# Kernel tuning notes

Measured on AMD Instinct MI355X. Metric: run time of the kernel, lower is better.

Reference implementation:

```python
import jax, jax.numpy as jnp
import numpy as np

EMB_DIM = 512
N_HEAD = 8
HEAD_DIM = EMB_DIM // N_HEAD
SEQ_LEN = 2048
BATCH = 4


def setup_inputs() -> dict:
    key = jax.random.key(0)
    k1, k2, k3 = jax.random.split(key, 3)
    emb = jax.random.normal(k1, (SEQ_LEN, BATCH, EMB_DIM), dtype=jnp.float32)
    # torch Linear weight layout: (out_features, in_features)
    W = jax.random.normal(k2, (3 * EMB_DIM, EMB_DIM), dtype=jnp.float32) * 0.02
    b = jax.random.normal(k3, (3 * EMB_DIM,), dtype=jnp.float32) * 0.02
    return {"emb": emb, "W": W, "b": b}


def reference(emb, W, b):
    L, B, E = emb.shape
    scaling = (E / N_HEAD) ** -0.5
    # qkv projection: (L, B, 3E)
    ft = jnp.einsum('lbe,oe->lbo', emb, W) + b
    # interleaved per-head qkv split, matching reshape(L, B*nh, -1).chunk(3, -1)
    ft = ft.reshape(L, B * N_HEAD, 3 * HEAD_DIM).transpose(1, 0, 2)  # (B*nh, L, 3*hd)
    q, k, v = jnp.split(ft, 3, axis=-1)  # each (B*nh, L, hd)
    # attention scores with value-based zero mask
    scores = jnp.einsum('bld,bmd->blm', q, k) * scaling  # (B*nh, L, L)
    mask = scores == 0
    scores = jnp.where(mask, -jnp.inf, scores)
    attn = jax.nn.softmax(scores, axis=-1)
    attn = jnp.where(mask, jnp.zeros((), attn.dtype), attn)
    out = jnp.einsum('blm,bmd->bld', attn, v)  # (B*nh, L, hd)
    out = out.transpose(1, 0, 2).reshape(L, B, E)
    return out
```

## Files before the change

kernel.cpp:

```cpp
#include <hip/hip_runtime.h>
#include <hip/hip_bf16.h>
#include <cstdint>
#include <math.h>


typedef __bf16 bf16x8 __attribute__((ext_vector_type(8)));
typedef float  f32x4  __attribute__((ext_vector_type(4)));
typedef float  f32x16 __attribute__((ext_vector_type(16)));
typedef unsigned int uint32x4 __attribute__((ext_vector_type(4)));

#define MFMA16(a, b, c) __builtin_amdgcn_mfma_f32_16x16x32_bf16(a, b, c, 0, 0, 0)
#define MFMA32(a, b, c) __builtin_amdgcn_mfma_f32_32x32x16_bf16(a, b, c, 0, 0, 0)

#define EXP2F(x) __builtin_amdgcn_exp2f(x)

#define QSCALE 0.18033688011112042f

enum {
  LSEQ = 2048,
  NBATCH = 4,
  EMB = 512,
  NHEAD = 8,
  HDIM = 64,
  NBH = NBATCH * NHEAD,
  MROWS = LSEQ * NBATCH,
  KDIM = EMB,
  NOUT = 3 * EMB
};

__device__ inline void gload_lds16(const void* g, void* l) {
  __builtin_amdgcn_global_load_lds(
      (__attribute__((address_space(1))) void*)(uintptr_t)g,
      (__attribute__((address_space(3))) void*)(uint32_t)(uintptr_t)l,
      16, 0, 0);
}

__device__ inline unsigned packbf(float a, float b) {
  unsigned short ua = __builtin_bit_cast(unsigned short, (__bf16)a);
  unsigned short ub = __builtin_bit_cast(unsigned short, (__bf16)b);
  return (unsigned)ua | ((unsigned)ub << 16);
}

__device__ inline bf16x8 frag_from(unsigned w0, unsigned w1, unsigned w2, unsigned w3) {
  uint32x4 v = {w0, w1, w2, w3};
  return __builtin_bit_cast(bf16x8, v);
}

__global__ __launch_bounds__(256) void cvt_bf16_kernel(const float* __restrict__ in,
                                                       __bf16* __restrict__ out,
                                                       int n8) {
  int i = blockIdx.x * 256 + threadIdx.x;
  if (i >= n8) return;
  const float4* p = (const float4*)in + (size_t)i * 2;
  float4 a = p[0], b = p[1];
  bf16x8 o;
  o[0] = (__bf16)a.x; o[1] = (__bf16)a.y; o[2] = (__bf16)a.z; o[3] = (__bf16)a.w;
  o[4] = (__bf16)b.x; o[5] = (__bf16)b.y; o[6] = (__bf16)b.z; o[7] = (__bf16)b.w;
  *(bf16x8*)(out + (size_t)i * 8) = o;
}

__global__ __launch_bounds__(256) void qkv_gemm_kernel(
    const __bf16* __restrict__ A, const __bf16* __restrict__ Bt,
    const float* __restrict__ bias,
    __bf16* __restrict__ Qh, __bf16* __restrict__ Kh, __bf16* __restrict__ Vth) {
  __shared__ __align__(16) __bf16 As[128 * 64];
  __shared__ __align__(16) __bf16 Bs[128 * 64];

  const int tid = threadIdx.x;
  const int wid = tid >> 6, lane = tid & 63;
  const int g = lane >> 4, lx = lane & 15;
  const int mtile = blockIdx.y, ntile = blockIdx.x;
  const int wm = (wid >> 1) * 64, wn = (wid & 1) * 64;

  const int lr = lane >> 3;
  const int lc = (lane & 7) * 8;

  f32x4 acc[4][4] = {};

  const int rowA0 = mtile * 128;
  const int rowB0 = ntile * 128;

  for (int k0 = 0; k0 < KDIM; k0 += 64) {
#pragma unroll
    for (int i = 0; i < 4; ++i) {
      int chunk = wid * 4 + i;
      gload_lds16(A + (size_t)(rowA0 + chunk * 8 + lr) * KDIM + k0 + lc,
                  As + chunk * 512);
      gload_lds16(Bt + (size_t)(rowB0 + chunk * 8 + lr) * KDIM + k0 + lc,
                  Bs + chunk * 512);
    }
    __syncthreads();
#pragma unroll
    for (int kk = 0; kk < 2; ++kk) {
      bf16x8 af[4], bfr[4];
#pragma unroll
      for (int t = 0; t < 4; ++t)
        af[t] = *(const bf16x8*)&As[(wm + t * 16 + lx) * 64 + kk * 32 + g * 8];
#pragma unroll
      for (int t = 0; t < 4; ++t)
        bfr[t] = *(const bf16x8*)&Bs[(wn + t * 16 + lx) * 64 + kk * 32 + g * 8];
#pragma unroll
      for (int mi = 0; mi < 4; ++mi)
#pragma unroll
        for (int ni = 0; ni < 4; ++ni)
          acc[mi][ni] = MFMA16(af[mi], bfr[ni], acc[mi][ni]);
    }
    __syncthreads();
  }

#pragma unroll
  for (int ni = 0; ni < 4; ++ni) {
    int o = ntile * 128 + wn + ni * 16 + lx;
    float bv = bias[o];
    unsigned h = (unsigned)o / 192u;
    unsigned w = (unsigned)o - h * 192u;
#pragma unroll
    for (int mi = 0; mi < 4; ++mi) {
#pragma unroll
      for (int r = 0; r < 4; ++r) {
        int m = mtile * 128 + wm + mi * 16 + g * 4 + r;
        int l = m >> 2, b = m & 3;
        float v = acc[mi][ni][r] + bv;
        int bh = b * NHEAD + (int)h;
        if (w < 64u) {
          Qh[((size_t)bh * LSEQ + l) * HDIM + w] = (__bf16)(v * QSCALE);
        } else if (w < 128u) {
          Kh[((size_t)bh * LSEQ + l) * HDIM + (w - 64u)] = (__bf16)v;
        } else {
          Vth[((size_t)bh * HDIM + (w - 128u)) * LSEQ + l] = (__bf16)v;
        }
      }
    }
  }
}

__global__ __launch_bounds__(512, 4) void attn_kernel(const __bf16* __restrict__ Qh,
                                                      const __bf16* __restrict__ Kh,
                                                      const __bf16* __restrict__ Vth,
                                                      float* __restrict__ out) {
  __shared__ __align__(16) __bf16 Ks[4][64 * 64];
  __shared__ __align__(16) __bf16 Vs[4][64 * 64];

  const int flat = blockIdx.x;
  const int sw = (flat & 7) * 64 + (flat >> 3);
  const int bh = sw >> 4, qt = sw & 15;
  const int tid = threadIdx.x, wid = tid >> 6, lane = tid & 63;
  const int pair = wid >> 1, role = wid & 1;
  const int ql = lane & 31, hi = lane >> 5;
  const int rb = ql & 7;

  const __bf16* Kb = Kh + (size_t)bh * (LSEQ * HDIM);
  const __bf16* Vb = Vth + (size_t)bh * (HDIM * LSEQ);

  const __bf16* Qp =
      Qh + ((size_t)bh * LSEQ + qt * 128 + pair * 32 + ql) * HDIM + hi * 8;
  bf16x8 qf[4];
#pragma unroll
  for (int s = 0; s < 4; ++s) qf[s] = *(const bf16x8*)(Qp + s * 16);

  const int w4 = wid & 3;
  const int tsel = wid >> 2;
  const int r8 = lane >> 3;
  const int colS = ((lane & 7) ^ r8) * 8;
  const __bf16* pK = Kb + (size_t)(w4 * 16 + r8) * HDIM + colS;
  const __bf16* pV = Vb + (size_t)(w4 * 16 + r8) * LSEQ + colS;

#define STAGE_SS(ss)                                                  \
  do {                                                                \
    int t_ = (2 * (ss) + tsel) & 31;                                  \
    int b_ = t_ & 3;                                                  \
    gload_lds16(pK + (size_t)t_ * (64 * HDIM), &Ks[b_][(w4 * 16) * 64]);      \
    gload_lds16(pK + (size_t)t_ * (64 * HDIM) + 512, &Ks[b_][(w4 * 16 + 8) * 64]); \
    gload_lds16(pV + t_ * 64, &Vs[b_][(w4 * 16) * 64]);               \
    gload_lds16(pV + t_ * 64 + 8 * LSEQ, &Vs[b_][(w4 * 16 + 8) * 64]); \
  } while (0)

  f32x16 ot[2] = {};
  f32x16 lacc = {};

  STAGE_SS(0);
  STAGE_SS(1);
  asm volatile("s_waitcnt vmcnt(4)" ::: "memory");
  __builtin_amdgcn_s_barrier();
  asm volatile("" ::: "memory");

  for (int s = 0; s < 16; ++s) {
    const int cur = (2 * s + role) & 3;

    f32x16 st[2] = {};
    __builtin_amdgcn_s_setprio(1);
#pragma unroll
    for (int kt = 0; kt < 2; ++kt) {
      const __bf16* kr = &Ks[cur][(kt * 32 + ql) * 64];
#pragma unroll
      for (int fs = 0; fs < 4; ++fs) {
        bf16x8 kf = *(const bf16x8*)(kr + (((2 * fs + hi) ^ rb) << 3));
        st[kt] = MFMA32(kf, qf[fs], st[kt]);
      }
    }
    __builtin_amdgcn_s_setprio(0);

#pragma unroll
    for (int r = 0; r < 16; ++r) {
      float e0 = EXP2F(st[0][r]);
      float e1 = EXP2F(st[1][r]);
      st[0][r] = e0;
      st[1][r] = e1;
      lacc[r] += e0 + e1;
    }

    bf16x8 pf[4];
#pragma unroll
    for (int kt = 0; kt < 2; ++kt)
#pragma unroll
      for (int h2 = 0; h2 < 2; ++h2) {
        unsigned a0 = packbf(st[kt][8 * h2 + 0], st[kt][8 * h2 + 1]);
        unsigned a1 = packbf(st[kt][8 * h2 + 2], st[kt][8 * h2 + 3]);
        unsigned a2 = packbf(st[kt][8 * h2 + 4], st[kt][8 * h2 + 5]);
        unsigned a3 = packbf(st[kt][8 * h2 + 6], st[kt][8 * h2 + 7]);
        asm("v_permlane32_swap_b32 %0, %1" : "+v"(a0), "+v"(a2));
        asm("v_permlane32_swap_b32 %0, %1" : "+v"(a1), "+v"(a3));
        pf[kt * 2 + h2] = frag_from(a0, a1, a2, a3);
      }

    __builtin_amdgcn_s_setprio(1);
#pragma unroll
    for (int dt = 0; dt < 2; ++dt) {
      const __bf16* vr = &Vs[cur][(dt * 32 + ql) * 64];
#pragma unroll
      for (int fs = 0; fs < 4; ++fs) {
        bf16x8 vf = *(const bf16x8*)(vr + (((2 * fs + hi) ^ rb) << 3));
        ot[dt] = MFMA32(vf, pf[fs], ot[dt]);
      }
    }
    __builtin_amdgcn_s_setprio(0);

    asm volatile("" ::: "memory");
    __builtin_amdgcn_s_barrier();
    asm volatile("" ::: "memory");
    STAGE_SS(s + 2);
    asm volatile("s_waitcnt vmcnt(4)" ::: "memory");
    __builtin_amdgcn_s_barrier();
    asm volatile("" ::: "memory");
  }
#undef STAGE_SS

  float ls = 0.f;
#pragma unroll
  for (int r = 0; r < 16; ++r) ls += lacc[r];
  ls += __shfl_xor(ls, 32);

  __syncthreads();
  float* stash_ot = (float*)&Ks[0][0];
  float* stash_ls = (float*)&Vs[0][0];
  float* myo = stash_ot + (wid * 64 + lane) * 16;
  f32x16 give = role ? ot[0] : ot[1];
#pragma unroll
  for (int g4 = 0; g4 < 4; ++g4) {
    float4 v4 = make_float4(give[4 * g4 + 0], give[4 * g4 + 1],
                            give[4 * g4 + 2], give[4 * g4 + 3]);
    *(float4*)(myo + 4 * g4) = v4;
  }
  stash_ls[wid * 64 + lane] = ls;
  __syncthreads();

  const float* po = stash_ot + ((wid ^ 1) * 64 + lane) * 16;
  f32x16 mine = role ? ot[1] : ot[0];
#pragma unroll
  for (int r = 0; r < 16; ++r) mine[r] += po[r];
  const float lst = ls + stash_ls[(wid ^ 1) * 64 + lane];
  const float inv = 1.f / lst;

  const int lq = qt * 128 + pair * 32 + ql;
  float* ob = out + (size_t)lq * (NBATCH * EMB) + (bh >> 3) * EMB + (bh & 7) * HDIM;
#pragma unroll
  for (int g4 = 0; g4 < 4; ++g4) {
    float4 v4 = make_float4(mine[4 * g4 + 0] * inv, mine[4 * g4 + 1] * inv,
                            mine[4 * g4 + 2] * inv, mine[4 * g4 + 3] * inv);
    *(float4*)(ob + role * 32 + g4 * 8 + hi * 4) = v4;
  }
}

extern "C" void kernel_launch(void* const* d_in, const int* in_sizes, int n_in,
                              void* d_out, int out_size, void* d_ws, size_t ws_size,
                              hipStream_t stream) {
  const float* emb = (const float*)d_in[0];
  const float* W = (const float*)d_in[1];
  const float* bias = (const float*)d_in[2];
  float* out = (float*)d_out;

  char* ws = (char*)d_ws;
  __bf16* embh = (__bf16*)(ws);
  __bf16* Wh   = (__bf16*)(ws + 8388608);
  __bf16* Qh   = (__bf16*)(ws + 9961472);
  __bf16* Kh   = (__bf16*)(ws + 18350080);
  __bf16* Vth  = (__bf16*)(ws + 26738688);

  cvt_bf16_kernel<<<dim3(MROWS * KDIM / 8 / 256), dim3(256), 0, stream>>>(emb, embh,
                                                                          MROWS * KDIM / 8);
  cvt_bf16_kernel<<<dim3(NOUT * KDIM / 8 / 256), dim3(256), 0, stream>>>(W, Wh,
                                                                         NOUT * KDIM / 8);
  qkv_gemm_kernel<<<dim3(NOUT / 128, MROWS / 128), dim3(256), 0, stream>>>(
      embh, Wh, bias, Qh, Kh, Vth);
  attn_kernel<<<dim3(NBH * (LSEQ / 128)), dim3(512), 0, stream>>>(Qh, Kh, Vth, out);
}
```

Before: 97.74 us.

## Give each wave private K/V half-tile LDS buffers and drop block barriers

The shared 4-deep K/V ring, which needed two block-wide barriers per iteration, is replaced by a private per-wave LDS region. Each role-wave stages its own 32-key half of the K and V tiles with per-wave vmcnt/lgkmcnt waits and no s_barrier. The loop now runs 32 half-tiles with one QK MFMA chain per step instead of 16 full tiles, and the next K and V loads are issued right after the current tile is consumed. This removes cross-wave synchronization, but the prefetch depth drops to a single buffer, so load latency may be less well hidden. Pairs of waves also load overlapping Q data independently.

```diff
diff --git a/kernel.cpp b/kernel.cpp
--- a/kernel.cpp
+++ b/kernel.cpp
@@ -138,8 +138,7 @@
                                                       const __bf16* __restrict__ Kh,
                                                       const __bf16* __restrict__ Vth,
                                                       float* __restrict__ out) {
-  __shared__ __align__(16) __bf16 Ks[4][64 * 64];
-  __shared__ __align__(16) __bf16 Vs[4][64 * 64];
+  __shared__ __align__(16) __bf16 SB[8][4096];
 
   const int flat = blockIdx.x;
   const int sw = (flat & 7) * 64 + (flat >> 3);
@@ -158,101 +157,106 @@
 #pragma unroll
   for (int s = 0; s < 4; ++s) qf[s] = *(const bf16x8*)(Qp + s * 16);
 
-  const int w4 = wid & 3;
-  const int tsel = wid >> 2;
-  const int r8 = lane >> 3;
-  const int colS = ((lane & 7) ^ r8) * 8;
-  const __bf16* pK = Kb + (size_t)(w4 * 16 + r8) * HDIM + colS;
-  const __bf16* pV = Vb + (size_t)(w4 * 16 + r8) * LSEQ + colS;
-
-#define STAGE_SS(ss)                                                  \
-  do {                                                                \
-    int t_ = (2 * (ss) + tsel) & 31;                                  \
-    int b_ = t_ & 3;                                                  \
-    gload_lds16(pK + (size_t)t_ * (64 * HDIM), &Ks[b_][(w4 * 16) * 64]);      \
-    gload_lds16(pK + (size_t)t_ * (64 * HDIM) + 512, &Ks[b_][(w4 * 16 + 8) * 64]); \
-    gload_lds16(pV + t_ * 64, &Vs[b_][(w4 * 16) * 64]);               \
-    gload_lds16(pV + t_ * 64 + 8 * LSEQ, &Vs[b_][(w4 * 16 + 8) * 64]); \
-  } while (0)
+  const int lr3 = lane >> 3;
+  const int ch = (lane & 7) ^ lr3;
+  const __bf16* srcK[4];
+  const __bf16* srcV[4];
+#pragma unroll
+  for (int c = 0; c < 4; ++c) {
+    srcK[c] = Kb + (size_t)(role * 32 + c * 8 + lr3) * HDIM + ch * 8;
+    srcV[c] = Vb + (size_t)((c * 8 + lr3) + (ch >> 2) * 32) * LSEQ + role * 32 +
+              (ch & 3) * 8;
+  }
+  __bf16* kbuf = &SB[wid][0];
+  __bf16* vbuf = &SB[wid][2048];
+
+#define STAGE_K(tn)                                                      \
+  {                                                                      \
+    _Pragma("unroll") for (int c = 0; c < 4; ++c)                        \
+        gload_lds16(srcK[c] + (size_t)(tn) * (64 * HDIM), kbuf + c * 512); \
+  }
+#define STAGE_V(tn)                                                      \
+  {                                                                      \
+    _Pragma("unroll") for (int c = 0; c < 4; ++c)                        \
+        gload_lds16(srcV[c] + (size_t)(tn) * 64, vbuf + c * 512);        \
+  }
+
+  int ko[4], vo[4];
+#pragma unroll
+  for (int fs = 0; fs < 4; ++fs) ko[fs] = ql * 64 + (((2 * fs + hi) ^ rb) << 3);
+#pragma unroll
+  for (int dt = 0; dt < 2; ++dt)
+#pragma unroll
+    for (int ks = 0; ks < 2; ++ks)
+      vo[dt * 2 + ks] = ql * 64 + (((dt * 4 + 2 * ks + hi) ^ rb) << 3);
 
   f32x16 ot[2] = {};
-  f32x16 lacc = {};
-
-  STAGE_SS(0);
-  STAGE_SS(1);
-  asm volatile("s_waitcnt vmcnt(4)" ::: "memory");
-  __builtin_amdgcn_s_barrier();
-  asm volatile("" ::: "memory");
-
-  for (int s = 0; s < 16; ++s) {
-    const int cur = (2 * s + role) & 3;
-
-    f32x16 st[2] = {};
+  float lacc[8] = {};
+
+  STAGE_K(0);
+  STAGE_V(0);
+
+  for (int t = 0; t < 32; ++t) {
+    asm volatile("s_waitcnt vmcnt(4)" ::: "memory");
+
+    f32x16 st = {};
     __builtin_amdgcn_s_setprio(1);
 #pragma unroll
-    for (int kt = 0; kt < 2; ++kt) {
-      const __bf16* kr = &Ks[cur][(kt * 32 + ql) * 64];
-#pragma unroll
-      for (int fs = 0; fs < 4; ++fs) {
-        bf16x8 kf = *(const bf16x8*)(kr + (((2 * fs + hi) ^ rb) << 3));
-        st[kt] = MFMA32(kf, qf[fs], st[kt]);
-      }
+    for (int fs = 0; fs < 4; ++fs) {
+      bf16x8 kf = *(const bf16x8*)(kbuf + ko[fs]);
+      st = MFMA32(kf, qf[fs], st);
     }
     __builtin_amdgcn_s_setprio(0);
 
+    asm volatile("s_waitcnt lgkmcnt(0)" ::: "memory");
+    const int tn = (t + 1) & 31;
+    STAGE_K(tn);
+
 #pragma unroll
     for (int r = 0; r < 16; ++r) {
-      float e0 = EXP2F(st[0][r]);
-      float e1 = EXP2F(st[1][r]);
-      st[0][r] = e0;
-      st[1][r] = e1;
-      lacc[r] += e0 + e1;
-    }
-
-    bf16x8 pf[4];
-#pragma unroll
-    for (int kt = 0; kt < 2; ++kt)
-#pragma unroll
-      for (int h2 = 0; h2 < 2; ++h2) {
-        unsigned a0 = packbf(st[kt][8 * h2 + 0], st[kt][8 * h2 + 1]);
-        unsigned a1 = packbf(st[kt][8 * h2 + 2], st[kt][8 * h2 + 3]);
-        unsigned a2 = packbf(st[kt][8 * h2 + 4], st[kt][8 * h2 + 5]);
-        unsigned a3 = packbf(st[kt][8 * h2 + 6], st[kt][8 * h2 + 7]);
-        asm("v_permlane32_swap_b32 %0, %1" : "+v"(a0), "+v"(a2));
-        asm("v_permlane32_swap_b32 %0, %1" : "+v"(a1), "+v"(a3));
-        pf[kt * 2 + h2] = frag_from(a0, a1, a2, a3);
-      }
+      float e = EXP2F(st[r]);
+      st[r] = e;
+      lacc[r & 7] += e;
+    }
+
+    unsigned b0 = packbf(st[0], st[1]), b1 = packbf(st[2], st[3]);
+    unsigned b2 = packbf(st[4], st[5]), b3 = packbf(st[6], st[7]);
+    unsigned b4 = packbf(st[8], st[9]), b5 = packbf(st[10], st[11]);
+    unsigned b6 = packbf(st[12], st[13]), b7 = packbf(st[14], st[15]);
+    asm("v_permlane32_swap_b32 %0, %1" : "+v"(b0), "+v"(b2));
+    asm("v_permlane32_swap_b32 %0, %1" : "+v"(b1), "+v"(b3));
+    asm("v_permlane32_swap_b32 %0, %1" : "+v"(b4), "+v"(b6));
+    asm("v_permlane32_swap_b32 %0, %1" : "+v"(b5), "+v"(b7));
+    bf16x8 pf0 = frag_from(b0, b1, b2, b3);
+    bf16x8 pf1 = frag_from(b4, b5, b6, b7);
+
+    asm volatile("s_waitcnt vmcnt(4)" ::: "memory");
 
     __builtin_amdgcn_s_setprio(1);
 #pragma unroll
     for (int dt = 0; dt < 2; ++dt) {
-      const __bf16* vr = &Vs[cur][(dt * 32 + ql) * 64];
-#pragma unroll
-      for (int fs = 0; fs < 4; ++fs) {
-        bf16x8 vf = *(const bf16x8*)(vr + (((2 * fs + hi) ^ rb) << 3));
-        ot[dt] = MFMA32(vf, pf[fs], ot[dt]);
-      }
+      bf16x8 v0 = *(const bf16x8*)(vbuf + vo[dt * 2 + 0]);
+      ot[dt] = MFMA32(v0, pf0, ot[dt]);
+      bf16x8 v1 = *(const bf16x8*)(vbuf + vo[dt * 2 + 1]);
+      ot[dt] = MFMA32(v1, pf1, ot[dt]);
     }
     __builtin_amdgcn_s_setprio(0);
 
-    asm volatile("" ::: "memory");
-    __builtin_amdgcn_s_barrier();
-    asm volatile("" ::: "memory");
-    STAGE_SS(s + 2);
-    asm volatile("s_waitcnt vmcnt(4)" ::: "memory");
-    __builtin_amdgcn_s_barrier();
-    asm volatile("" ::: "memory");
-  }
-#undef STAGE_SS
+    asm volatile("s_waitcnt lgkmcnt(0)" ::: "memory");
+    STAGE_V(tn);
+  }
+#undef STAGE_K
+#undef STAGE_V
 
   float ls = 0.f;
 #pragma unroll
-  for (int r = 0; r < 16; ++r) ls += lacc[r];
+  for (int r = 0; r < 8; ++r) ls += lacc[r];
   ls += __shfl_xor(ls, 32);
 
+  asm volatile("s_waitcnt vmcnt(0) lgkmcnt(0)" ::: "memory");
   __syncthreads();
-  float* stash_ot = (float*)&Ks[0][0];
-  float* stash_ls = (float*)&Vs[0][0];
+  float* stash_ot = (float*)&SB[0][0];
+  float* stash_ls = stash_ot + 8192;
   float* myo = stash_ot + (wid * 64 + lane) * 16;
   f32x16 give = role ? ot[0] : ot[1];
 #pragma unroll
```

New measurement: 104.8 us. +7.2%, slower.
